# Kernel tuning notes

Measured on AMD Instinct MI355X. Metric: run time of the kernel, lower is better.

## Reference

```python
import jax, jax.numpy as jnp
import numpy as np

N = 100000
F_IN = 128
H = 64
E = 3200000


def setup_inputs() -> dict:
    key = jax.random.key(0)
    ks = jax.random.split(key, 10)
    x = jax.random.normal(ks[0], (N, F_IN), dtype=jnp.float32)
    edge_index = jax.random.randint(ks[1], (2, E), 0, N, dtype=jnp.int64)
    hidden_state = jax.random.normal(ks[2], (1, N, H), dtype=jnp.float32)
    # GCNConv params (glorot-ish scale)
    W_gcn = jax.random.normal(ks[3], (F_IN, H), dtype=jnp.float32) / np.sqrt(F_IN)
    b_gcn = jnp.zeros((H,), dtype=jnp.float32)
    # torch.nn.GRU params, layout [3H, in] with gate order (r, z, n)
    s = 1.0 / np.sqrt(H)
    W_ih = jax.random.uniform(ks[4], (3 * H, H), dtype=jnp.float32, minval=-s, maxval=s)
    W_hh = jax.random.uniform(ks[5], (3 * H, H), dtype=jnp.float32, minval=-s, maxval=s)
    b_ih = jax.random.uniform(ks[6], (3 * H,), dtype=jnp.float32, minval=-s, maxval=s)
    b_hh = jax.random.uniform(ks[7], (3 * H,), dtype=jnp.float32, minval=-s, maxval=s)
    return {"x": x, "edge_index": edge_index, "hidden_state": hidden_state,
            "W_gcn": W_gcn, "b_gcn": b_gcn,
            "W_ih": W_ih, "W_hh": W_hh, "b_ih": b_ih, "b_hh": b_hh}


def gcn_conv(x, edge_index, W, b):
    n = x.shape[0]
    # add self-loops (PyG GCNConv default)
    loops = jnp.arange(n, dtype=edge_index.dtype)
    row = jnp.concatenate([edge_index[0], loops])  # source
    col = jnp.concatenate([edge_index[1], loops])  # target
    # symmetric normalization: deg over targets with unit edge weights
    deg = jax.ops.segment_sum(jnp.ones_like(col, dtype=x.dtype), col, num_segments=n)
    dis = jnp.where(deg > 0, jax.lax.rsqrt(deg), 0.0)
    norm = dis[row] * dis[col]  # (E+N,)
    xt = x @ W  # (N, H) transform first, then aggregate
    msg = norm[:, None] * xt[row]  # (E+N, H)
    out = jax.ops.segment_sum(msg, col, num_segments=n)
    return out + b


def gru_step(x, h, W_ih, W_hh, b_ih, b_hh):
    # single-step torch GRU, gate order (r, z, n)
    gi = x @ W_ih.T + b_ih  # (N, 3H)
    gh = h @ W_hh.T + b_hh
    i_r, i_z, i_n = jnp.split(gi, 3, axis=-1)
    h_r, h_z, h_n = jnp.split(gh, 3, axis=-1)
    r = jax.nn.sigmoid(i_r + h_r)
    z = jax.nn.sigmoid(i_z + h_z)
    n = jnp.tanh(i_n + r * h_n)
    return (1.0 - z) * n + z * h


def reference(x, edge_index, hidden_state, W_gcn, b_gcn, W_ih, W_hh, b_ih, b_hh):
    g = jax.nn.relu(gcn_conv(x, edge_index, W_gcn, b_gcn))  # (N, H)
    h_new = gru_step(g, hidden_state[0], W_ih, W_hh, b_ih, b_hh)  # (N, H)
    return h_new, h_new[None]  # (out, new_hidden_state)
```

## Files before the change

kernel.cpp:

```cpp
#include <hip/hip_runtime.h>
#include <cmath>

constexpr int NN  = 100000;
constexpr int FIN = 128;
constexpr int HH  = 64;
constexpr int NE  = 3200000;
constexpr int NB  = (NN + 255) / 256;
constexpr int NFB  = NB;
constexpr int PCAP = 10240;

typedef __attribute__((ext_vector_type(8))) short short8;
typedef __attribute__((ext_vector_type(4))) float f32x4;

__device__ __forceinline__ ushort f2bf(float x) {
    unsigned u = __float_as_uint(x);
    u += 0x7FFF + ((u >> 16) & 1);
    return (ushort)(u >> 16);
}
__device__ __forceinline__ float bf2f(ushort h) {
    return __uint_as_float(((unsigned)h) << 16);
}
__device__ __forceinline__ unsigned pack2(float a, float b) {
    return (unsigned)f2bf(a) | ((unsigned)f2bf(b) << 16);
}

__global__ void __launch_bounds__(256) k_part(const int* __restrict__ ei,
                                              int* __restrict__ gcnt,
                                              int* __restrict__ pairs) {
    __shared__ int lcnt[NFB];
    __shared__ int lbase[NFB];
    int t = threadIdx.x;
    for (int i = t; i < NFB; i += 256) lcnt[i] = 0;
    __syncthreads();

    long long base = (long long)blockIdx.x * 8192;
    int4 r4[8], c4[8];
    int nv[8];
#pragma unroll
    for (int s = 0; s < 8; ++s) {
        long long e = base + s * 1024 + t * 4;
        if (e < NE) {
            r4[s] = ((const int4*)(ei))[e >> 2];
            c4[s] = ((const int4*)(ei + NE))[e >> 2];
            nv[s] = 1;
            atomicAdd(&lcnt[c4[s].x >> 8], 1);
            atomicAdd(&lcnt[c4[s].y >> 8], 1);
            atomicAdd(&lcnt[c4[s].z >> 8], 1);
            atomicAdd(&lcnt[c4[s].w >> 8], 1);
        } else {
            nv[s] = 0;
        }
    }
    __syncthreads();
    for (int i = t; i < NFB; i += 256) {
        int c = lcnt[i];
        lbase[i] = c ? atomicAdd(&gcnt[i], c) : 0;
        lcnt[i] = 0;
    }
    __syncthreads();
#pragma unroll
    for (int s = 0; s < 8; ++s) {
        if (!nv[s]) continue;
        int rr[4] = {r4[s].x, r4[s].y, r4[s].z, r4[s].w};
        int cc[4] = {c4[s].x, c4[s].y, c4[s].z, c4[s].w};
#pragma unroll
        for (int k = 0; k < 4; ++k) {
            int b   = cc[k] >> 8;
            int p   = atomicAdd(&lcnt[b], 1);
            int pos = lbase[b] + p;
            if (pos < PCAP) pairs[b * PCAP + pos] = (rr[k] << 8) | (cc[k] & 255);
        }
    }
}

__global__ void __launch_bounds__(512) k_csr(const int* __restrict__ pairs,
                                             const int* __restrict__ gcnt,
                                             int* __restrict__ deg,
                                             int* __restrict__ rowptr,
                                             float* __restrict__ dis,
                                             int* __restrict__ csr) {
    __shared__ int sg[512];
    __shared__ int ldeg[256];
    __shared__ int lrp[512];
    __shared__ int lcur[256];
    __shared__ int lcsr[PCAP];
    int f = blockIdx.x;
    int t = threadIdx.x;
    sg[t] = (t < f) ? gcnt[t] : 0;
    if (t < 256) ldeg[t] = 0;
    __syncthreads();
    for (int off = 256; off > 0; off >>= 1) {
        if (t < off) sg[t] += sg[t + off];
        __syncthreads();
    }
    int base = sg[0];
    int cnt  = min(gcnt[f], PCAP);
    int n0   = f * 256;
    const int* pb = pairs + f * PCAP;
    for (int i = t; i < cnt; i += 512) atomicAdd(&ldeg[pb[i] & 255], 1);
    __syncthreads();
    int v = (t < 256) ? ldeg[t] : 0;
    lrp[t] = v;
    __syncthreads();
    for (int off = 1; off < 256; off <<= 1) {
        int add = (t >= off) ? lrp[t - off] : 0;
        __syncthreads();
        lrp[t] += add;
        __syncthreads();
    }
    int excl = lrp[t] - v;
    if (t < 256) {
        if (n0 + t < NN) {
            deg[n0 + t]    = v;
            rowptr[n0 + t] = base + excl;
            dis[n0 + t]    = rsqrtf((float)(v + 1));
        }
        lcur[t] = excl;
    }
    __syncthreads();
    for (int i = t; i < cnt; i += 512) {
        int e = pb[i];
        int p = atomicAdd(&lcur[e & 255], 1);
        lcsr[p] = e >> 8;
    }
    __syncthreads();
    for (int i = t; i < cnt; i += 512) csr[base + i] = lcsr[i];
}

__global__ void __launch_bounds__(256) k_xt(const float* __restrict__ x,
                                            const ushort* __restrict__ wgx,
                                            const float* __restrict__ dis,
                                            ushort* __restrict__ xtb) {
    __shared__ ushort Ahi[64 * 136];
    __shared__ ushort Alo[64 * 136];
    __shared__ float sdis[64];
    const ushort* GXhi = wgx;
    const ushort* GXlo = wgx + 64 * 128;
    int t  = threadIdx.x;
    int r0 = blockIdx.x * 64;
    if (t < 64) sdis[t] = (r0 + t < NN) ? dis[r0 + t] : 0.f;
    unsigned* Ahi32 = (unsigned*)Ahi;
    unsigned* Alo32 = (unsigned*)Alo;
#pragma unroll
    for (int s = 0; s < 8; ++s) {
        int idx = t + 256 * s;
        int nd  = idx >> 5;
        int kq  = idx & 31;
        bool ok = (r0 + nd) < NN;
        float4 v = ok ? ((const float4*)(x + (size_t)(r0 + nd) * FIN))[kq]
                      : make_float4(0.f, 0.f, 0.f, 0.f);
        int b2 = nd * 68 + kq * 2;
        float hx = bf2f(f2bf(v.x)), hy = bf2f(f2bf(v.y));
        float hz = bf2f(f2bf(v.z)), hw = bf2f(f2bf(v.w));
        Ahi32[b2]     = pack2(v.x, v.y);
        Ahi32[b2 + 1] = pack2(v.z, v.w);
        Alo32[b2]     = pack2(v.x - hx, v.y - hy);
        Alo32[b2 + 1] = pack2(v.z - hz, v.w - hw);
    }
    __syncthreads();

    int lane = t & 63, w = t >> 6, l15 = lane & 15;
    int kbase = (lane >> 4) * 8;
    int j = w * 16 + l15;
    f32x4 acc[4];
#pragma unroll
    for (int m = 0; m < 4; ++m) acc[m] = (f32x4){0.f, 0.f, 0.f, 0.f};
    short8 bh[4], bl[4];
#pragma unroll
    for (int ks = 0; ks < 4; ++ks) {
        bh[ks] = *(const short8*)(GXhi + j * 128 + ks * 32 + kbase);
        bl[ks] = *(const short8*)(GXlo + j * 128 + ks * 32 + kbase);
    }
#pragma unroll
    for (int mt = 0; mt < 4; ++mt) {
        int abase = (mt * 16 + l15) * 136 + kbase;
#pragma unroll
        for (int ks = 0; ks < 4; ++ks) {
            short8 ah = *(const short8*)&Ahi[abase + ks * 32];
            short8 al = *(const short8*)&Alo[abase + ks * 32];
            acc[mt] = __builtin_amdgcn_mfma_f32_16x16x32_bf16(ah, bh[ks], acc[mt], 0, 0, 0);
            acc[mt] = __builtin_amdgcn_mfma_f32_16x16x32_bf16(al, bh[ks], acc[mt], 0, 0, 0);
            acc[mt] = __builtin_amdgcn_mfma_f32_16x16x32_bf16(ah, bl[ks], acc[mt], 0, 0, 0);
        }
    }
    __syncthreads();
#pragma unroll
    for (int mt = 0; mt < 4; ++mt) {
#pragma unroll
        for (int reg = 0; reg < 4; ++reg) {
            int row = mt * 16 + (lane >> 4) * 4 + reg;
            Alo[row * 64 + j] = f2bf(sdis[row] * acc[mt][reg]);
        }
    }
    __syncthreads();
    const uint4* src = (const uint4*)Alo;
    uint4* dst = (uint4*)(xtb + (size_t)r0 * HH);
#pragma unroll
    for (int s = 0; s < 2; ++s) {
        int u   = t + 256 * s;
        int row = u >> 3;
        if (r0 + row < NN) dst[u] = src[u];
    }
}

__global__ void __launch_bounds__(256) k_gather(const int* __restrict__ csr,
                                                const int* __restrict__ rowptr,
                                                const int* __restrict__ deg,
                                                const float* __restrict__ dis,
                                                const ushort* __restrict__ xtb,
                                                const float* __restrict__ bg,
                                                float* __restrict__ g) {
    __shared__ int lid[4][64];
    int t    = threadIdx.x;
    int lane = t & 63;
    int w    = t >> 6;
    int n    = blockIdx.x * 4 + w;
    int r = lane >> 3;
    int q = lane & 7;
    float acc[8] = {0.f, 0.f, 0.f, 0.f, 0.f, 0.f, 0.f, 0.f};
    float dn  = dis[n];
    int start = rowptr[n];
    int cnt   = deg[n];
    for (int c0 = 0; c0 < cnt; c0 += 64) {
        int m = min(64, cnt - c0);
        if (lane < m) lid[w][lane] = csr[start + c0 + lane];
        int i = r;
        for (; i + 8 < m; i += 16) {
            int s0 = lid[w][i];
            int s1 = lid[w][i + 8];
            short8 v0 = ((const short8*)(xtb + (size_t)s0 * HH))[q];
            short8 v1 = ((const short8*)(xtb + (size_t)s1 * HH))[q];
#pragma unroll
            for (int j = 0; j < 8; ++j) acc[j] += bf2f((ushort)v0[j]);
#pragma unroll
            for (int j = 0; j < 8; ++j) acc[j] += bf2f((ushort)v1[j]);
        }
        if (i < m) {
            int s0 = lid[w][i];
            short8 v0 = ((const short8*)(xtb + (size_t)s0 * HH))[q];
#pragma unroll
            for (int j = 0; j < 8; ++j) acc[j] += bf2f((ushort)v0[j]);
        }
    }
#pragma unroll
    for (int j = 0; j < 8; ++j) {
        acc[j] += __shfl_xor(acc[j], 8, 64);
        acc[j] += __shfl_xor(acc[j], 16, 64);
        acc[j] += __shfl_xor(acc[j], 32, 64);
    }
    if (r == 0) {
        short8 xs = ((const short8*)(xtb + (size_t)n * HH))[q];
        float4 b0 = ((const float4*)bg)[q * 2];
        float4 b1 = ((const float4*)bg)[q * 2 + 1];
        float bb[8] = {b0.x, b0.y, b0.z, b0.w, b1.x, b1.y, b1.z, b1.w};
        float res[8];
#pragma unroll
        for (int j = 0; j < 8; ++j)
            res[j] = fmaxf(fmaf(dn, acc[j] + bf2f((ushort)xs[j]), bb[j]), 0.f);
        float4* go = (float4*)(g + (size_t)n * HH + q * 8);
        go[0] = make_float4(res[0], res[1], res[2], res[3]);
        go[1] = make_float4(res[4], res[5], res[6], res[7]);
    }
}

__global__ void k_wprep(const float* __restrict__ Wih, const float* __restrict__ Whh,
                        const float* __restrict__ Wg, ushort* __restrict__ bsp,
                        int* __restrict__ gcnt) {
    ushort* Bhi  = bsp;
    ushort* Blo  = bsp + 192 * 128;
    ushort* BShi = bsp + 2 * 192 * 128;
    ushort* BSlo = BShi + 64 * 64;
    ushort* GXhi = BSlo + 64 * 64;
    ushort* GXlo = GXhi + 64 * 128;
    int i = blockIdx.x * 256 + threadIdx.x;
    if (i < NFB) gcnt[i] = 0;
    if (i < 192 * 128) {
        int j = i >> 7, k = i & 127;
        float wv = (k < 64) ? Wih[j * 64 + k] : Whh[j * 64 + (k - 64)];
        ushort hi = f2bf(wv);
        Bhi[i] = hi;
        Blo[i] = f2bf(wv - bf2f(hi));
    }
    if (i < 64 * 64) {
        int j = i >> 6, k = i & 63;
        float wv = Whh[(128 + j) * 64 + k];
        ushort hi = f2bf(wv);
        BShi[i] = hi;
        BSlo[i] = f2bf(wv - bf2f(hi));
    }
    if (i < 64 * 128) {
        int j = i >> 7, k = i & 127;
        float wv = Wg[k * HH + j];
        ushort hi = f2bf(wv);
        GXhi[i] = hi;
        GXlo[i] = f2bf(wv - bf2f(hi));
    }
}

__global__ void __launch_bounds__(256) k_gru(
    const float* __restrict__ gbuf, const float* __restrict__ hprev,
    const ushort* __restrict__ bsp,
    const float* __restrict__ bih, const float* __restrict__ bhh,
    float* __restrict__ out) {
    __shared__ ushort Ahi[64 * 136];
    __shared__ ushort Alo[64 * 136];
    const ushort* Bhi  = bsp;
    const ushort* Blo  = bsp + 192 * 128;
    const ushort* BShi = bsp + 2 * 192 * 128;
    const ushort* BSlo = BShi + 64 * 64;

    int t  = threadIdx.x;
    int n0 = blockIdx.x * 64;

    unsigned* Ahi32 = (unsigned*)Ahi;
    unsigned* Alo32 = (unsigned*)Alo;
#pragma unroll
    for (int s = 0; s < 4; ++s) {
        int idx = t + 256 * s;
        int nd  = idx >> 4;
        int kq  = idx & 15;
        bool ok = (n0 + nd) < NN;
        float4 vg = ok ? ((const float4*)(gbuf  + (size_t)(n0 + nd) * HH))[kq]
                       : make_float4(0.f, 0.f, 0.f, 0.f);
        float4 vh = ok ? ((const float4*)(hprev + (size_t)(n0 + nd) * HH))[kq]
                       : make_float4(0.f, 0.f, 0.f, 0.f);
        int bg2 = nd * 68 + kq * 2;
        int bh2 = bg2 + 32;
        float ghx = bf2f(f2bf(vg.x)), ghy = bf2f(f2bf(vg.y));
        float ghz = bf2f(f2bf(vg.z)), ghw = bf2f(f2bf(vg.w));
        float hhx = bf2f(f2bf(vh.x)), hhy = bf2f(f2bf(vh.y));
        float hhz = bf2f(f2bf(vh.z)), hhw = bf2f(f2bf(vh.w));
        Ahi32[bg2]     = pack2(vg.x, vg.y);
        Ahi32[bg2 + 1] = pack2(vg.z, vg.w);
        Alo32[bg2]     = pack2(vg.x - ghx, vg.y - ghy);
        Alo32[bg2 + 1] = pack2(vg.z - ghz, vg.w - ghw);
        Ahi32[bh2]     = pack2(vh.x, vh.y);
        Ahi32[bh2 + 1] = pack2(vh.z, vh.w);
        Alo32[bh2]     = pack2(vh.x - hhx, vh.y - hhy);
        Alo32[bh2 + 1] = pack2(vh.z - hhz, vh.w - hhw);
    }
    __syncthreads();

    int lane  = t & 63;
    int w     = t >> 6;
    int l15   = lane & 15;
    int kbase = (lane >> 4) * 8;

    f32x4 acc[4][4];
#pragma unroll
    for (int a = 0; a < 4; ++a)
#pragma unroll
        for (int m = 0; m < 4; ++m) acc[a][m] = (f32x4){0.f, 0.f, 0.f, 0.f};

#pragma unroll
    for (int g = 0; g < 3; ++g) {
        int brow = (w + 4 * g) * 16 + l15;
        short8 bh[4], bl[4];
#pragma unroll
        for (int ks = 0; ks < 4; ++ks) {
            bh[ks] = *(const short8*)(Bhi + brow * 128 + ks * 32 + kbase);
            bl[ks] = *(const short8*)(Blo + brow * 128 + ks * 32 + kbase);
        }
#pragma unroll
        for (int mt = 0; mt < 4; ++mt) {
            int abase = (mt * 16 + l15) * 136 + kbase;
#pragma unroll
            for (int ks = 0; ks < 4; ++ks) {
                short8 ah = *(const short8*)&Ahi[abase + ks * 32];
                short8 al = *(const short8*)&Alo[abase + ks * 32];
                acc[g][mt] = __builtin_amdgcn_mfma_f32_16x16x32_bf16(ah, bh[ks], acc[g][mt], 0, 0, 0);
                acc[g][mt] = __builtin_amdgcn_mfma_f32_16x16x32_bf16(al, bh[ks], acc[g][mt], 0, 0, 0);
                acc[g][mt] = __builtin_amdgcn_mfma_f32_16x16x32_bf16(ah, bl[ks], acc[g][mt], 0, 0, 0);
            }
        }
    }
    {
        int brow = w * 16 + l15;
        short8 bh[2], bl[2];
#pragma unroll
        for (int ks = 0; ks < 2; ++ks) {
            bh[ks] = *(const short8*)(BShi + brow * 64 + ks * 32 + kbase);
            bl[ks] = *(const short8*)(BSlo + brow * 64 + ks * 32 + kbase);
        }
#pragma unroll
        for (int mt = 0; mt < 4; ++mt) {
            int abase = (mt * 16 + l15) * 136 + 64 + kbase;
#pragma unroll
            for (int ks = 0; ks < 2; ++ks) {
                short8 ah = *(const short8*)&Ahi[abase + ks * 32];
                short8 al = *(const short8*)&Alo[abase + ks * 32];
                acc[3][mt] = __builtin_amdgcn_mfma_f32_16x16x32_bf16(ah, bh[ks], acc[3][mt], 0, 0, 0);
                acc[3][mt] = __builtin_amdgcn_mfma_f32_16x16x32_bf16(al, bh[ks], acc[3][mt], 0, 0, 0);
                acc[3][mt] = __builtin_amdgcn_mfma_f32_16x16x32_bf16(ah, bl[ks], acc[3][mt], 0, 0, 0);
            }
        }
    }

    int j = 16 * w + l15;
    float br  = bih[j] + bhh[j];
    float bz  = bih[HH + j] + bhh[HH + j];
    float bin = bih[2 * HH + j];
    float bhn = bhh[2 * HH + j];
#pragma unroll
    for (int mt = 0; mt < 4; ++mt) {
#pragma unroll
        for (int reg = 0; reg < 4; ++reg) {
            int row  = mt * 16 + (lane >> 4) * 4 + reg;
            int node = n0 + row;
            if (node < NN) {
                float S1 = acc[0][mt][reg];
                float S2 = acc[1][mt][reg];
                float S3 = acc[2][mt][reg];
                float Hn = acc[3][mt][reg];
                float r  = __builtin_amdgcn_rcpf(1.f + __expf(-(S1 + br)));
                float z  = __builtin_amdgcn_rcpf(1.f + __expf(-(S2 + bz)));
                float na = (S3 - Hn + bin) + r * (Hn + bhn);
                float e2 = __expf(2.f * na);
                float nv = fmaf(-2.f, __builtin_amdgcn_rcpf(1.f + e2), 1.f);
                int lidx = row * 136 + 64 + j;
                float h  = bf2f(Ahi[lidx]) + bf2f(Alo[lidx]);
                float o  = (1.f - z) * nv + z * h;
                out[(size_t)node * HH + j] = o;
                out[(size_t)NN * HH + (size_t)node * HH + j] = o;
            }
        }
    }
}

extern "C" void kernel_launch(void* const* d_in, const int* in_sizes, int n_in,
                              void* d_out, int out_size, void* d_ws, size_t ws_size,
                              hipStream_t stream) {
    const float* x   = (const float*)d_in[0];
    const int*   ei  = (const int*)d_in[1];
    const float* hs  = (const float*)d_in[2];
    const float* Wg  = (const float*)d_in[3];
    const float* bg  = (const float*)d_in[4];
    const float* Wih = (const float*)d_in[5];
    const float* Whh = (const float*)d_in[6];
    const float* bih = (const float*)d_in[7];
    const float* bhh = (const float*)d_in[8];
    float* out = (float*)d_out;

    char* ws = (char*)d_ws;
    int*    pairs  = (int*)   (ws);
    ushort* xtb    = (ushort*)(ws);
    float*  gbuf   = (float*) (ws + 16400000);
    int*    csr    = (int*)   (ws + 42000000);
    int*    deg    = (int*)   (ws + 54800000);
    int*    rowptr = (int*)   (ws + 55200000);
    float*  dis    = (float*) (ws + 55600000);
    ushort* wsplit = (ushort*)(ws + 56000000);
    int*    gcnt   = (int*)   (ws + 56200000);

    hipLaunchKernelGGL(k_wprep, dim3(96), dim3(256), 0, stream, Wih, Whh, Wg, wsplit, gcnt);
    hipLaunchKernelGGL(k_part,  dim3((NE + 8191) / 8192), dim3(256), 0, stream, ei, gcnt, pairs);
    hipLaunchKernelGGL(k_csr,   dim3(NFB), dim3(512), 0, stream,
                       pairs, gcnt, deg, rowptr, dis, csr);
    hipLaunchKernelGGL(k_xt,    dim3((NN + 63) / 64), dim3(256), 0, stream,
                       x, wsplit + 2 * 192 * 128 + 2 * 64 * 64, dis, xtb);
    hipLaunchKernelGGL(k_gather, dim3(NN / 4), dim3(256), 0, stream,
                       csr, rowptr, deg, dis, xtb, bg, gbuf);
    hipLaunchKernelGGL(k_gru,   dim3((NN + 63) / 64), dim3(256), 0, stream,
                       gbuf, hs, wsplit, bih, bhh, out);
}
```

Baseline: 309.2 us.

## Split gather into four feature-slice passes over a column-partitioned xt layout

k_xt now writes the transformed features as four planar slices of 16 bf16 columns per node instead of row-major 64 columns. The gather runs as four separate launches, each aggregating one 16-column slice, so each pass's working set (about 3.2 MB) is more likely to stay cache-resident during the random neighbor reads. In exchange, the CSR index lists are re-read four times, there are four launches, and each neighbor fetch is only a 32-byte load.

```diff
diff --git a/kernel.cpp b/kernel.cpp
--- a/kernel.cpp
+++ b/kernel.cpp
@@ -193,30 +193,37 @@
         }
     }
     __syncthreads();
-    const uint4* src = (const uint4*)Alo;
-    uint4* dst = (uint4*)(xtb + (size_t)r0 * HH);
+    const uint4* src4 = (const uint4*)Alo;
 #pragma unroll
     for (int s = 0; s < 2; ++s) {
         int u   = t + 256 * s;
-        int row = u >> 3;
-        if (r0 + row < NN) dst[u] = src[u];
-    }
-}
-
-__global__ void __launch_bounds__(256) k_gather(const int* __restrict__ csr,
-                                                const int* __restrict__ rowptr,
-                                                const int* __restrict__ deg,
-                                                const float* __restrict__ dis,
-                                                const ushort* __restrict__ xtb,
-                                                const float* __restrict__ bg,
-                                                float* __restrict__ g) {
+        int p   = u >> 7;
+        int rem = u & 127;
+        int nd  = rem >> 1;
+        int h   = rem & 1;
+        if (r0 + nd < NN) {
+            uint4 val = src4[nd * 8 + p * 2 + h];
+            ((uint4*)xtb)[(size_t)p * NN * 2 + (size_t)(r0 + nd) * 2 + h] = val;
+        }
+    }
+}
+
+__global__ void __launch_bounds__(256) k_gat(const int* __restrict__ csr,
+                                             const int* __restrict__ rowptr,
+                                             const int* __restrict__ deg,
+                                             const float* __restrict__ dis,
+                                             const ushort* __restrict__ xtb,
+                                             const float* __restrict__ bg,
+                                             float* __restrict__ g,
+                                             int pass) {
     __shared__ int lid[4][64];
     int t    = threadIdx.x;
     int lane = t & 63;
     int w    = t >> 6;
     int n    = blockIdx.x * 4 + w;
-    int r = lane >> 3;
-    int q = lane & 7;
+    int el   = lane >> 1;
+    int half = lane & 1;
+    const ushort* xp = xtb + (size_t)pass * NN * 16;
     float acc[8] = {0.f, 0.f, 0.f, 0.f, 0.f, 0.f, 0.f, 0.f};
     float dn  = dis[n];
     int start = rowptr[n];
@@ -224,40 +231,31 @@
     for (int c0 = 0; c0 < cnt; c0 += 64) {
         int m = min(64, cnt - c0);
         if (lane < m) lid[w][lane] = csr[start + c0 + lane];
-        int i = r;
-        for (; i + 8 < m; i += 16) {
-            int s0 = lid[w][i];
-            int s1 = lid[w][i + 8];
-            short8 v0 = ((const short8*)(xtb + (size_t)s0 * HH))[q];
-            short8 v1 = ((const short8*)(xtb + (size_t)s1 * HH))[q];
-#pragma unroll
-            for (int j = 0; j < 8; ++j) acc[j] += bf2f((ushort)v0[j]);
-#pragma unroll
-            for (int j = 0; j < 8; ++j) acc[j] += bf2f((ushort)v1[j]);
-        }
-        if (i < m) {
-            int s0 = lid[w][i];
-            short8 v0 = ((const short8*)(xtb + (size_t)s0 * HH))[q];
-#pragma unroll
-            for (int j = 0; j < 8; ++j) acc[j] += bf2f((ushort)v0[j]);
+        for (int i = el; i < m; i += 32) {
+            int src = lid[w][i];
+            short8 v = *(const short8*)(xp + (size_t)src * 16 + half * 8);
+#pragma unroll
+            for (int j = 0; j < 8; ++j) acc[j] += bf2f((ushort)v[j]);
         }
     }
 #pragma unroll
     for (int j = 0; j < 8; ++j) {
+        acc[j] += __shfl_xor(acc[j], 2, 64);
+        acc[j] += __shfl_xor(acc[j], 4, 64);
         acc[j] += __shfl_xor(acc[j], 8, 64);
         acc[j] += __shfl_xor(acc[j], 16, 64);
         acc[j] += __shfl_xor(acc[j], 32, 64);
     }
-    if (r == 0) {
-        short8 xs = ((const short8*)(xtb + (size_t)n * HH))[q];
-        float4 b0 = ((const float4*)bg)[q * 2];
-        float4 b1 = ((const float4*)bg)[q * 2 + 1];
+    if (el == 0) {
+        short8 xs = *(const short8*)(xp + (size_t)n * 16 + half * 8);
+        float4 b0 = ((const float4*)bg)[pass * 4 + half * 2];
+        float4 b1 = ((const float4*)bg)[pass * 4 + half * 2 + 1];
         float bb[8] = {b0.x, b0.y, b0.z, b0.w, b1.x, b1.y, b1.z, b1.w};
         float res[8];
 #pragma unroll
         for (int j = 0; j < 8; ++j)
             res[j] = fmaxf(fmaf(dn, acc[j] + bf2f((ushort)xs[j]), bb[j]), 0.f);
-        float4* go = (float4*)(g + (size_t)n * HH + q * 8);
+        float4* go = (float4*)(g + (size_t)n * HH + pass * 16 + half * 8);
         go[0] = make_float4(res[0], res[1], res[2], res[3]);
         go[1] = make_float4(res[4], res[5], res[6], res[7]);
     }
@@ -458,8 +456,9 @@
                        pairs, gcnt, deg, rowptr, dis, csr);
     hipLaunchKernelGGL(k_xt,    dim3((NN + 63) / 64), dim3(256), 0, stream,
                        x, wsplit + 2 * 192 * 128 + 2 * 64 * 64, dis, xtb);
-    hipLaunchKernelGGL(k_gather, dim3(NN / 4), dim3(256), 0, stream,
-                       csr, rowptr, deg, dis, xtb, bg, gbuf);
+    for (int p = 0; p < 4; ++p)
+        hipLaunchKernelGGL(k_gat, dim3(NN / 4), dim3(256), 0, stream,
+                           csr, rowptr, deg, dis, xtb, bg, gbuf, p);
     hipLaunchKernelGGL(k_gru,   dim3((NN + 63) / 64), dim3(256), 0, stream,
                        gbuf, hs, wsplit, bih, bhh, out);
 }
```

After: 442.6 us. +43.1%, slower.
